# Performance work log

Hardware: AMD Instinct MI355X
Metric: run time of the kernel (lower is better)

Reference implementation:

```python
import jax, jax.numpy as jnp
import numpy as np

N = 100_000      # nodes
E = 1_600_000    # edges
F_IN = 4         # num_features
H = 128          # hidden_channels
C = 5            # num_classes
G = 256          # graphs in batch


def setup_inputs() -> dict:
    key = jax.random.key(0)
    ks = jax.random.split(key, 14)
    x = jax.random.normal(ks[0], (N, F_IN), dtype=jnp.float32)
    edge_index = jax.random.randint(ks[1], (2, E), 0, N, dtype=jnp.int64)
    batch = jnp.sort(jax.random.randint(ks[2], (N,), 0, G, dtype=jnp.int64))
    def lin(k, fan_in, fan_out):
        kw, kb = jax.random.split(k)
        s = 1.0 / np.sqrt(fan_in)
        W = jax.random.uniform(kw, (fan_in, fan_out), jnp.float32, -s, s)
        b = jax.random.uniform(kb, (fan_out,), jnp.float32, -s, s)
        return W, b
    W1, b1 = lin(ks[3], F_IN, H)
    W2, b2 = lin(ks[4], H, H)
    W3, b3 = lin(ks[5], H, H)
    W4, b4 = lin(ks[6], H, H)
    Wl, bl = lin(ks[7], H, C)
    return {"x": x, "edge_index": edge_index, "batch": batch,
            "W1": W1, "b1": b1, "W2": W2, "b2": b2,
            "W3": W3, "b3": b3, "W4": W4, "b4": b4,
            "Wl": Wl, "bl": bl}


def reference(x, edge_index, batch, W1, b1, W2, b2, W3, b3, W4, b4, Wl, bl):
    n = x.shape[0]
    loop = jnp.arange(n, dtype=edge_index.dtype)
    src = jnp.concatenate([edge_index[0], loop])  # [E+N], with self-loops
    dst = jnp.concatenate([edge_index[1], loop])
    # symmetric normalization on A + I (PyG GCNConv default)
    deg = jax.ops.segment_sum(jnp.ones_like(dst, dtype=x.dtype), dst, num_segments=n)
    dinv = deg ** -0.5  # deg >= 1 thanks to self-loops
    coef = dinv[src] * dinv[dst]  # per-edge norm [E+N]

    def conv(h, W, b):
        h = h @ W                               # [N, H]
        msg = h[src] * coef[:, None]            # gather + scale [E+N, H]
        return jax.ops.segment_sum(msg, dst, num_segments=n) + b

    h = jax.nn.relu(conv(x, W1, b1))
    h = jax.nn.relu(conv(h, W2, b2))
    h = jax.nn.relu(conv(h, W3, b3))
    h = jax.nn.relu(conv(h, W4, b4))

    # global_mean_pool over graph ids
    counts = jax.ops.segment_sum(jnp.ones((n,), h.dtype), batch, num_segments=G)
    pooled = jax.ops.segment_sum(h, batch, num_segments=G)
    pooled = pooled / jnp.maximum(counts, 1.0)[:, None]  # [G, H]

    return jax.nn.sigmoid(pooled @ Wl + bl)  # [G, C]
```

## Files before the change

kernel.cpp:

```cpp
#include <hip/hip_runtime.h>
#include <hip/hip_fp8.h>
#include <math.h>

#define N_NODES 100000
#define N_EDGES 1600000
#define F_IN    4
#define HID     128
#define N_CLS   5
#define N_GRAPH 256
#define POOL_SEG 8

#define BSHIFT   9
#define BSIZE    512
#define NBUK     196
#define NCHUNK   200
#define CHUNK    8000

typedef _Float16 f16;
typedef _Float16 f16x2 __attribute__((ext_vector_type(2)));
typedef _Float16 f16x8 __attribute__((ext_vector_type(8)));
typedef float f32x4 __attribute__((ext_vector_type(4)));

__device__ __forceinline__ float rec_coef(unsigned r) {
    return (float)__builtin_bit_cast(_Float16, (unsigned short)(r & 0x7FFFu));
}

__device__ __forceinline__ float2 fp8x2_to_f32x2(unsigned short raw) {
    __hip_fp8x2_e4m3 t;
    t.__x = raw;
    return static_cast<float2>(t);
}

__device__ __forceinline__ void fma8(float c, uint2 v, float* acc) {
    float2 p0 = fp8x2_to_f32x2((unsigned short)(v.x & 0xFFFFu));
    float2 p1 = fp8x2_to_f32x2((unsigned short)(v.x >> 16));
    float2 p2 = fp8x2_to_f32x2((unsigned short)(v.y & 0xFFFFu));
    float2 p3 = fp8x2_to_f32x2((unsigned short)(v.y >> 16));
    acc[0] = fmaf(c, p0.x, acc[0]); acc[1] = fmaf(c, p0.y, acc[1]);
    acc[2] = fmaf(c, p1.x, acc[2]); acc[3] = fmaf(c, p1.y, acc[3]);
    acc[4] = fmaf(c, p2.x, acc[4]); acc[5] = fmaf(c, p2.y, acc[5]);
    acc[6] = fmaf(c, p3.x, acc[6]); acc[7] = fmaf(c, p3.y, acc[7]);
}

__global__ __launch_bounds__(256) void k_bc(const int* __restrict__ dst, int* __restrict__ C) {
    __shared__ int cnt[NBUK];
    int t = threadIdx.x;
    if (t < NBUK) cnt[t] = 0;
    __syncthreads();
    int base = blockIdx.x * CHUNK;
#pragma unroll
    for (int it = 0; it < 32; ++it) {
        int idx = it * 256 + t;
        if (idx < CHUNK) atomicAdd(&cnt[dst[base + idx] >> BSHIFT], 1);
    }
    __syncthreads();
    if (t < NBUK) C[blockIdx.x * NBUK + t] = cnt[t];
}

__global__ __launch_bounds__(256) void k_bscan(const int* __restrict__ C, int* __restrict__ Off,
                                               int* __restrict__ bbase) {
    __shared__ int s[256];
    int b = threadIdx.x;
    int tot = 0;
    if (b < NBUK) {
        for (int c = 0; c < NCHUNK; ++c) {
            Off[c * NBUK + b] = tot;
            tot += C[c * NBUK + b];
        }
    }
    s[b] = (b < NBUK) ? tot : 0;
    __syncthreads();
    for (int off = 1; off < 256; off <<= 1) {
        int v = (b >= off) ? s[b - off] : 0;
        __syncthreads();
        s[b] += v;
        __syncthreads();
    }
    if (b < NBUK) bbase[b] = s[b] - tot;
    if (b == 0) bbase[NBUK] = N_EDGES;
}

__global__ __launch_bounds__(256) void k_scatter(const int* __restrict__ src, const int* __restrict__ dst,
                                                 const int* __restrict__ Off, const int* __restrict__ bbase,
                                                 unsigned* __restrict__ bkt) {
    __shared__ int cur[NBUK];
    int t = threadIdx.x;
    if (t < NBUK) cur[t] = bbase[t] + Off[blockIdx.x * NBUK + t];
    __syncthreads();
    int base = blockIdx.x * CHUNK;
#pragma unroll
    for (int it = 0; it < 32; ++it) {
        int idx = it * 256 + t;
        if (idx < CHUNK) {
            int s = src[base + idx], d = dst[base + idx];
            int b = d >> BSHIFT;
            int p = atomicAdd(&cur[b], 1);
            bkt[p] = ((unsigned)s << BSHIFT) | (unsigned)(d & (BSIZE - 1));
        }
    }
}

__global__ __launch_bounds__(256) void k_hist2(const unsigned* __restrict__ bkt,
                                               const int* __restrict__ bbase,
                                               int* __restrict__ deg, float* __restrict__ dinv,
                                               int* __restrict__ padTot) {
    __shared__ int hist[BSIZE];
    __shared__ int tot;
    int t = threadIdx.x, b = blockIdx.x;
    hist[t] = 0; hist[t + 256] = 0;
    if (t == 0) tot = 0;
    __syncthreads();
    int s0 = bbase[b], s1 = bbase[b + 1];
    for (int e = s0 + t; e < s1; e += 256) atomicAdd(&hist[bkt[e] & (BSIZE - 1)], 1);
    __syncthreads();
    int loc = 0;
#pragma unroll
    for (int h = 0; h < 2; ++h) {
        int l = t + h * 256;
        int node = b * BSIZE + l;
        int d = hist[l];
        if (node < N_NODES) {
            deg[node] = d;
            dinv[node] = rsqrtf((float)d + 1.0f);
        }
        loc += (d + 15) >> 4;
    }
    atomicAdd(&tot, loc);
    __syncthreads();
    if (t == 0) padTot[b] = tot << 4;
}

__global__ __launch_bounds__(256) void k_pscan(const int* __restrict__ padTot, int* __restrict__ padBase,
                                               int* __restrict__ rowptrP) {
    __shared__ int s[256];
    int b = threadIdx.x;
    int v = (b < NBUK) ? padTot[b] : 0;
    s[b] = v;
    __syncthreads();
    for (int off = 1; off < 256; off <<= 1) {
        int u = (b >= off) ? s[b - off] : 0;
        __syncthreads();
        s[b] += u;
        __syncthreads();
    }
    if (b < NBUK) padBase[b] = s[b] - v;
    if (b == 0) {
        padBase[NBUK] = s[NBUK - 1];
        rowptrP[N_NODES] = s[NBUK - 1];
    }
}

__global__ __launch_bounds__(256) void k_local2(const unsigned* __restrict__ bkt,
                                                const int* __restrict__ bbase,
                                                const int* __restrict__ deg,
                                                const float* __restrict__ dinv,
                                                const int* __restrict__ padBase,
                                                int* __restrict__ rowptrP,
                                                unsigned* __restrict__ edges) {
    __shared__ int sc[BSIZE];
    __shared__ int cur[BSIZE];
    __shared__ float dv[BSIZE];
    int t = threadIdx.x, b = blockIdx.x;
    int base = padBase[b];
    int n0 = b * BSIZE + t, n1 = n0 + 256;
    int d0 = (n0 < N_NODES) ? deg[n0] : 0;
    int d1 = (n1 < N_NODES) ? deg[n1] : 0;
    int p0 = ((d0 + 15) >> 4) << 4;
    int p1 = ((d1 + 15) >> 4) << 4;
    sc[t] = p0; sc[t + 256] = p1;
    dv[t] = (n0 < N_NODES) ? dinv[n0] : 0.f;
    dv[t + 256] = (n1 < N_NODES) ? dinv[n1] : 0.f;
    __syncthreads();
    for (int off = 1; off < BSIZE; off <<= 1) {
        int i0 = t, i1 = t + 256;
        int v0 = (i0 >= off) ? sc[i0 - off] : 0;
        int v1 = (i1 >= off) ? sc[i1 - off] : 0;
        __syncthreads();
        sc[i0] += v0; sc[i1] += v1;
        __syncthreads();
    }
    int off0 = base + sc[t] - p0;
    int off1 = base + sc[t + 256] - p1;
    if (n0 < N_NODES) rowptrP[n0] = off0;
    if (n1 < N_NODES) rowptrP[n1] = off1;
    cur[t] = off0; cur[t + 256] = off1;
    int padT = sc[BSIZE - 1];
    for (int i = base + t; i < base + padT; i += 256) edges[i] = 0;
    __syncthreads();
    int s0 = bbase[b], s1 = bbase[b + 1];
    for (int e = s0 + t; e < s1; e += 256) {
        unsigned r = bkt[e];
        int dl = (int)(r & (BSIZE - 1));
        int s = (int)(r >> BSHIFT);
        int p = atomicAdd(&cur[dl], 1);
        float c = dv[dl] * dinv[s];
        unsigned short cb = __builtin_bit_cast(unsigned short, (f16)c);
        edges[p] = ((unsigned)s << 15) | (unsigned)(cb & 0x7FFFu);
    }
}

__global__ __launch_bounds__(256) void k_aggxg(const float4* __restrict__ x,
                                               const int* __restrict__ rowptrP,
                                               const unsigned* __restrict__ edges,
                                               const float* __restrict__ dinv,
                                               const float* __restrict__ W1, const float* __restrict__ b1,
                                               unsigned* __restrict__ hA ) {
    __shared__ float4 sx[256];
    __shared__ float sW[4 * HID];
    __shared__ float sb[HID];
    int tid = threadIdx.x;
    sW[tid] = W1[tid];
    sW[tid + 256] = W1[tid + 256];
    if (tid < HID) sb[tid] = b1[tid];

    int i = blockIdx.x * 256 + tid;
    float4 agg = make_float4(0.f, 0.f, 0.f, 0.f);
    if (i < N_NODES) {
        float di = dinv[i];
        float4 xv = x[i];
        float c0 = di * di;
        agg.x = c0 * xv.x; agg.y = c0 * xv.y; agg.z = c0 * xv.z; agg.w = c0 * xv.w;
        int beg = rowptrP[i], end = rowptrP[i + 1];
        for (int e = beg; e < end; ++e) {
            unsigned r = edges[e];
            float c = rec_coef(r);
            float4 v = x[r >> 15];
            agg.x = fmaf(c, v.x, agg.x); agg.y = fmaf(c, v.y, agg.y);
            agg.z = fmaf(c, v.z, agg.z); agg.w = fmaf(c, v.w, agg.w);
        }
    }
    sx[tid] = agg;
    __syncthreads();

    int node0 = blockIdx.x * 256;
#pragma unroll
    for (int it = 0; it < 32; ++it) {
        int id = it * 256 + tid;
        int n = id >> 5;
        int g = id & 31;
        int node = node0 + n;
        if (node >= N_NODES) continue;
        float4 a = sx[n];
        float c[4];
#pragma unroll
        for (int j = 0; j < 4; ++j) {
            int col = g * 4 + j;
            float v = sb[col];
            v = fmaf(a.x, sW[col],           v);
            v = fmaf(a.y, sW[HID + col],     v);
            v = fmaf(a.z, sW[2 * HID + col], v);
            v = fmaf(a.w, sW[3 * HID + col], v);
            c[j] = fmaxf(v, 0.0f);
        }
        unsigned lo = __hip_fp8x2_e4m3(make_float2(c[0], c[1])).__x;
        unsigned hi = __hip_fp8x2_e4m3(make_float2(c[2], c[3])).__x;
        hA[node * 32 + g] = lo | (hi << 16);
    }
}

__global__ __launch_bounds__(256) void k_agg8p(const unsigned* __restrict__ h8,
                                               const int* __restrict__ rowptrP,
                                               const unsigned* __restrict__ edges,
                                               const float* __restrict__ dinv,
                                               f16* __restrict__ out) {
    int node = blockIdx.x * 4 + (threadIdx.x >> 6);
    if (node >= N_NODES) return;
    int lane = threadIdx.x & 63;
    int g = lane >> 4;
    int l = lane & 15;
    int beg = rowptrP[node], end = rowptrP[node + 1];

    float acc[8];
    {
        float di = dinv[node];
        float c0 = (g == 0) ? di * di : 0.0f;
        uint2 v = *(const uint2*)(h8 + (size_t)node * 32 + l * 2);
        float2 p0 = fp8x2_to_f32x2((unsigned short)(v.x & 0xFFFFu));
        float2 p1 = fp8x2_to_f32x2((unsigned short)(v.x >> 16));
        float2 p2 = fp8x2_to_f32x2((unsigned short)(v.y & 0xFFFFu));
        float2 p3 = fp8x2_to_f32x2((unsigned short)(v.y >> 16));
        acc[0] = c0 * p0.x; acc[1] = c0 * p0.y;
        acc[2] = c0 * p1.x; acc[3] = c0 * p1.y;
        acc[4] = c0 * p2.x; acc[5] = c0 * p2.y;
        acc[6] = c0 * p3.x; acc[7] = c0 * p3.y;
    }

    for (int e = beg; e < end; e += 16) {
        unsigned rec16 = edges[e + l];
#pragma unroll
        for (int i = 0; i < 4; ++i) {
            unsigned rec = __shfl(rec16, i * 4 + g, 64);
            float c = rec_coef(rec);
            uint2 v = *(const uint2*)(h8 + (size_t)(rec >> 15) * 32 + l * 2);
            fma8(c, v, acc);
        }
    }

#pragma unroll
    for (int j = 0; j < 8; ++j) {
        acc[j] += __shfl_xor(acc[j], 16, 64);
        acc[j] += __shfl_xor(acc[j], 32, 64);
    }
    if (lane < 16) {
        f16x8 o;
#pragma unroll
        for (int j = 0; j < 8; ++j) o[j] = (f16)acc[j];
        *(f16x8*)(out + (size_t)node * HID + l * 8) = o;
    }
}

__global__ __launch_bounds__(256) void k_packW3(const float* __restrict__ W2, const float* __restrict__ W3,
                                                const float* __restrict__ W4, f16* __restrict__ Wp) {
    int idx = blockIdx.x * 256 + threadIdx.x;
    int which = idx >> 14;
    int r = idx & 16383;
    const float* W = (which == 0) ? W2 : (which == 1) ? W3 : W4;
    int j  = r & 7;
    int L  = (r >> 3) & 63;
    int ks = (r >> 9) & 3;
    int ct = r >> 11;
    int k = ks * 32 + (L >> 4) * 8 + j;
    int n = ct * 16 + (L & 15);
    Wp[idx] = (f16)W[k * HID + n];
}

template <bool FP8OUT>
__global__ __launch_bounds__(256) void k_gemm_mfma(const f16* __restrict__ A, const f16* __restrict__ Wp,
                                                   const float* __restrict__ bias, void* __restrict__ outv) {
    int wave = threadIdx.x >> 6;
    int lane = threadIdx.x & 63;
    int row0 = blockIdx.x * 64 + wave * 16;
    if (row0 >= N_NODES) return;
    int m = lane & 15;
    int q = lane >> 4;
    const f16* Arow = A + (size_t)(row0 + m) * HID + q * 8;

    f32x4 acc[8];
#pragma unroll
    for (int t = 0; t < 8; ++t) acc[t] = (f32x4){0.f, 0.f, 0.f, 0.f};

#pragma unroll
    for (int ks = 0; ks < 4; ++ks) {
        f16x8 a = *(const f16x8*)(Arow + ks * 32);
#pragma unroll
        for (int t = 0; t < 8; ++t) {
            f16x8 b = *(const f16x8*)(Wp + ((size_t)(t * 4 + ks) * 64 + lane) * 8);
            acc[t] = __builtin_amdgcn_mfma_f32_16x16x32_f16(a, b, acc[t], 0, 0, 0);
        }
    }

    int orow = row0 + q * 4;
#pragma unroll
    for (int t = 0; t < 8; ++t) {
        float bb = bias[t * 16 + m];
#pragma unroll
        for (int r = 0; r < 4; ++r) {
            float val = fmaxf(acc[t][r] + bb, 0.0f);
            if constexpr (FP8OUT) {
                __hip_fp8_e4m3* out8 = (__hip_fp8_e4m3*)outv;
                out8[(size_t)(orow + r) * HID + t * 16 + m] = __hip_fp8_e4m3(val);
            } else {
                f16* out = (f16*)outv;
                out[(size_t)(orow + r) * HID + t * 16 + m] = (f16)val;
            }
        }
    }
}

__device__ __forceinline__ int lower_bound_batch(const int* __restrict__ batch, int val) {
    int lo = 0, hi = N_NODES;
    while (lo < hi) { int m = (lo + hi) >> 1; if (batch[m] < val) lo = m + 1; else hi = m; }
    return lo;
}

__global__ __launch_bounds__(128) void k_pool1(const f16* __restrict__ h, const int* __restrict__ batch,
                                               float* __restrict__ partials) {
    int g = blockIdx.x / POOL_SEG;
    int s = blockIdx.x % POOL_SEG;
    int f = threadIdx.x;
    int beg = lower_bound_batch(batch, g);
    int end = lower_bound_batch(batch, g + 1);
    int len = end - beg;
    int sb = beg + (int)(((long long)len * s) / POOL_SEG);
    int se = beg + (int)(((long long)len * (s + 1)) / POOL_SEG);
    float acc = 0.0f;
    for (int i = sb; i < se; ++i) acc += (float)h[i * HID + f];
    partials[(size_t)blockIdx.x * HID + f] = acc;
}

__global__ __launch_bounds__(128) void k_pool2h(const float* __restrict__ partials,
                                                const int* __restrict__ batch,
                                                const float* __restrict__ Wl, const float* __restrict__ bl,
                                                float* __restrict__ out) {
    __shared__ float sp[HID];
    int g = blockIdx.x;
    int f = threadIdx.x;
    float acc = 0.0f;
#pragma unroll
    for (int s = 0; s < POOL_SEG; ++s)
        acc += partials[(size_t)(g * POOL_SEG + s) * HID + f];
    int beg = lower_bound_batch(batch, g);
    int end = lower_bound_batch(batch, g + 1);
    sp[f] = acc / fmaxf((float)(end - beg), 1.0f);
    __syncthreads();
    if (f < N_CLS) {
        float v = bl[f];
        for (int k = 0; k < HID; ++k) v = fmaf(sp[k], Wl[k * N_CLS + f], v);
        out[g * N_CLS + f] = 1.0f / (1.0f + expf(-v));
    }
}

extern "C" void kernel_launch(void* const* d_in, const int* in_sizes, int n_in,
                              void* d_out, int out_size, void* d_ws, size_t ws_size,
                              hipStream_t stream) {
    const float* x     = (const float*)d_in[0];
    const int*   ei    = (const int*)d_in[1];
    const int*   batch = (const int*)d_in[2];
    const float* W1 = (const float*)d_in[3];  const float* b1 = (const float*)d_in[4];
    const float* W2 = (const float*)d_in[5];  const float* b2 = (const float*)d_in[6];
    const float* W3 = (const float*)d_in[7];  const float* b3 = (const float*)d_in[8];
    const float* W4 = (const float*)d_in[9];  const float* b4 = (const float*)d_in[10];
    const float* Wl = (const float*)d_in[11]; const float* bl = (const float*)d_in[12];
    float* out = (float*)d_out;

    const size_t EPAD = (size_t)N_EDGES + (size_t)N_NODES * 16;

    char* p = (char*)d_ws;
    auto alloc = [&](size_t bytes) { char* r = p; p += (bytes + 255) & ~(size_t)255; return (void*)r; };
    int*      C       = (int*)     alloc((size_t)NCHUNK * NBUK * 4);
    int*      Off     = (int*)     alloc((size_t)NCHUNK * NBUK * 4);
    int*      bbase   = (int*)     alloc((size_t)(NBUK + 1) * 4);
    int*      padTot  = (int*)     alloc((size_t)NBUK * 4);
    int*      padBase = (int*)     alloc((size_t)(NBUK + 1) * 4);
    unsigned* bkt     = (unsigned*)alloc((size_t)N_EDGES * 4);
    int*      deg     = (int*)     alloc((size_t)N_NODES * 4);
    int*      rowptrP = (int*)     alloc((size_t)(N_NODES + 1) * 4);
    float*    dinv    = (float*)   alloc((size_t)N_NODES * 4);
    unsigned* edges   = (unsigned*)alloc(EPAD * 4);
    unsigned* hA      = (unsigned*)alloc((size_t)N_NODES * HID);
    f16*      hB      = (f16*)     alloc((size_t)N_NODES * HID * 2);
    f16*      h4      = (f16*)     alloc((size_t)N_NODES * HID * 2);
    float*    parts   = (float*)   alloc((size_t)N_GRAPH * POOL_SEG * HID * 4);
    f16*      Wp      = (f16*)     alloc((size_t)3 * HID * HID * 2);
    f16*      Wp2 = Wp;
    f16*      Wp3 = Wp + HID * HID;
    f16*      Wp4 = Wp + 2 * HID * HID;

    const int* srcv = ei;
    const int* dstv = ei + N_EDGES;

    const int nb = (N_NODES + 255) / 256;

    k_bc     <<<NCHUNK, 256, 0, stream>>>(dstv, C);
    k_bscan  <<<1, 256, 0, stream>>>(C, Off, bbase);
    k_scatter<<<NCHUNK, 256, 0, stream>>>(srcv, dstv, Off, bbase, bkt);
    k_hist2  <<<NBUK, 256, 0, stream>>>(bkt, bbase, deg, dinv, padTot);
    k_pscan  <<<1, 256, 0, stream>>>(padTot, padBase, rowptrP);
    k_local2 <<<NBUK, 256, 0, stream>>>(bkt, bbase, deg, dinv, padBase, rowptrP, edges);

    k_packW3<<<192, 256, 0, stream>>>(W2, W3, W4, Wp);

    k_aggxg<<<nb, 256, 0, stream>>>((const float4*)x, rowptrP, edges, dinv, W1, b1, hA);

    const int ggrid = (N_NODES + 63) / 64;
    k_agg8p<<<N_NODES / 4, 256, 0, stream>>>(hA, rowptrP, edges, dinv, hB);
    k_gemm_mfma<true ><<<ggrid, 256, 0, stream>>>(hB, Wp2, b2, hA);
    k_agg8p<<<N_NODES / 4, 256, 0, stream>>>(hA, rowptrP, edges, dinv, hB);
    k_gemm_mfma<true ><<<ggrid, 256, 0, stream>>>(hB, Wp3, b3, hA);
    k_agg8p<<<N_NODES / 4, 256, 0, stream>>>(hA, rowptrP, edges, dinv, hB);
    k_gemm_mfma<false><<<ggrid, 256, 0, stream>>>(hB, Wp4, b4, h4);

    k_pool1 <<<N_GRAPH * POOL_SEG, 128, 0, stream>>>(h4, batch, parts);
    k_pool2h<<<N_GRAPH, 128, 0, stream>>>(parts, batch, Wl, bl, out);
}
```

Measured before the change: 377.0 us.

## Fuse GCN aggregation with MFMA GEMM per 16-node block via swizzled LDS

Each hidden layer's sparse aggregation is merged with the following 128x128 MFMA GEMM. A 1024-thread block aggregates 16 nodes (one wave per node) into an XOR-swizzled LDS tile, then 8 waves run the GEMM and write the fp8 or f16 output directly. This removes the fp16 intermediate round trip through global memory and three kernel launches. The first-layer aggregation now uses 16 lanes per node with shuffle reductions instead of one thread per node. The gather address math is also simplified. In exchange, half the waves sit idle during the GEMM phase and the large blocks may limit occupancy.

```diff
diff --git a/kernel.cpp b/kernel.cpp
--- a/kernel.cpp
+++ b/kernel.cpp
@@ -199,48 +199,54 @@
     }
 }
 
-__global__ __launch_bounds__(256) void k_aggxg(const float4* __restrict__ x,
+__global__ __launch_bounds__(256) void k_aggx1(const float4* __restrict__ x,
                                                const int* __restrict__ rowptrP,
                                                const unsigned* __restrict__ edges,
                                                const float* __restrict__ dinv,
                                                const float* __restrict__ W1, const float* __restrict__ b1,
-                                               unsigned* __restrict__ hA ) {
-    __shared__ float4 sx[256];
+                                               unsigned* __restrict__ hA) {
+    __shared__ float4 sxa[16];
     __shared__ float sW[4 * HID];
     __shared__ float sb[HID];
-    int tid = threadIdx.x;
-    sW[tid] = W1[tid];
-    sW[tid + 256] = W1[tid + 256];
-    if (tid < HID) sb[tid] = b1[tid];
-
-    int i = blockIdx.x * 256 + tid;
-    float4 agg = make_float4(0.f, 0.f, 0.f, 0.f);
-    if (i < N_NODES) {
-        float di = dinv[i];
-        float4 xv = x[i];
+    int t = threadIdx.x;
+    sW[t] = W1[t];
+    sW[t + 256] = W1[t + 256];
+    if (t < HID) sb[t] = b1[t];
+    int grp = t >> 4;
+    int l = t & 15;
+    int node = blockIdx.x * 16 + grp;
+    int beg = rowptrP[node], end = rowptrP[node + 1];
+    float ax = 0.f, ay = 0.f, az = 0.f, aw = 0.f;
+    for (int e = beg + l; e < end; e += 16) {
+        unsigned r = edges[e];
+        float c = rec_coef(r);
+        float4 v = x[r >> 15];
+        ax = fmaf(c, v.x, ax); ay = fmaf(c, v.y, ay);
+        az = fmaf(c, v.z, az); aw = fmaf(c, v.w, aw);
+    }
+#pragma unroll
+    for (int off = 1; off < 16; off <<= 1) {
+        ax += __shfl_xor(ax, off, 64);
+        ay += __shfl_xor(ay, off, 64);
+        az += __shfl_xor(az, off, 64);
+        aw += __shfl_xor(aw, off, 64);
+    }
+    if (l == 0) {
+        float di = dinv[node];
         float c0 = di * di;
-        agg.x = c0 * xv.x; agg.y = c0 * xv.y; agg.z = c0 * xv.z; agg.w = c0 * xv.w;
-        int beg = rowptrP[i], end = rowptrP[i + 1];
-        for (int e = beg; e < end; ++e) {
-            unsigned r = edges[e];
-            float c = rec_coef(r);
-            float4 v = x[r >> 15];
-            agg.x = fmaf(c, v.x, agg.x); agg.y = fmaf(c, v.y, agg.y);
-            agg.z = fmaf(c, v.z, agg.z); agg.w = fmaf(c, v.w, agg.w);
-        }
-    }
-    sx[tid] = agg;
-    __syncthreads();
-
-    int node0 = blockIdx.x * 256;
-#pragma unroll
-    for (int it = 0; it < 32; ++it) {
-        int id = it * 256 + tid;
+        float4 xv = x[node];
+        sxa[grp] = make_float4(fmaf(c0, xv.x, ax), fmaf(c0, xv.y, ay),
+                               fmaf(c0, xv.z, az), fmaf(c0, xv.w, aw));
+    }
+    __syncthreads();
+
+    int node0 = blockIdx.x * 16;
+#pragma unroll
+    for (int it = 0; it < 2; ++it) {
+        int id = it * 256 + t;
         int n = id >> 5;
         int g = id & 31;
-        int node = node0 + n;
-        if (node >= N_NODES) continue;
-        float4 a = sx[n];
+        float4 a = sxa[n];
         float c[4];
 #pragma unroll
         for (int j = 0; j < 4; ++j) {
@@ -254,27 +260,33 @@
         }
         unsigned lo = __hip_fp8x2_e4m3(make_float2(c[0], c[1])).__x;
         unsigned hi = __hip_fp8x2_e4m3(make_float2(c[2], c[3])).__x;
-        hA[node * 32 + g] = lo | (hi << 16);
-    }
-}
-
-__global__ __launch_bounds__(256) void k_agg8p(const unsigned* __restrict__ h8,
-                                               const int* __restrict__ rowptrP,
-                                               const unsigned* __restrict__ edges,
-                                               const float* __restrict__ dinv,
-                                               f16* __restrict__ out) {
-    int node = blockIdx.x * 4 + (threadIdx.x >> 6);
-    if (node >= N_NODES) return;
+        hA[(node0 + n) * 32 + g] = lo | (hi << 16);
+    }
+}
+
+template <bool FP8OUT>
+__global__ __launch_bounds__(1024, 8) void k_aggemm8(const unsigned* __restrict__ h8,
+                                                     const int* __restrict__ rowptrP,
+                                                     const unsigned* __restrict__ edges,
+                                                     const float* __restrict__ dinv,
+                                                     const f16* __restrict__ Wp,
+                                                     const float* __restrict__ bias,
+                                                     void* __restrict__ outv) {
+    __shared__ f16 S[16 * HID];
+    int wave = threadIdx.x >> 6;
     int lane = threadIdx.x & 63;
+    int node0 = blockIdx.x * 16;
+    int node = node0 + wave;
     int g = lane >> 4;
     int l = lane & 15;
     int beg = rowptrP[node], end = rowptrP[node + 1];
+    const char* hp = (const char*)h8 + l * 8;
 
     float acc[8];
     {
         float di = dinv[node];
         float c0 = (g == 0) ? di * di : 0.0f;
-        uint2 v = *(const uint2*)(h8 + (size_t)node * 32 + l * 2);
+        uint2 v = *(const uint2*)(hp + ((size_t)node << 7));
         float2 p0 = fp8x2_to_f32x2((unsigned short)(v.x & 0xFFFFu));
         float2 p1 = fp8x2_to_f32x2((unsigned short)(v.x >> 16));
         float2 p2 = fp8x2_to_f32x2((unsigned short)(v.y & 0xFFFFu));
@@ -291,7 +303,7 @@
         for (int i = 0; i < 4; ++i) {
             unsigned rec = __shfl(rec16, i * 4 + g, 64);
             float c = rec_coef(rec);
-            uint2 v = *(const uint2*)(h8 + (size_t)(rec >> 15) * 32 + l * 2);
+            uint2 v = *(const uint2*)(hp + ((rec >> 8) & 0xFFFFFF80u));
             fma8(c, v, acc);
         }
     }
@@ -305,7 +317,34 @@
         f16x8 o;
 #pragma unroll
         for (int j = 0; j < 8; ++j) o[j] = (f16)acc[j];
-        *(f16x8*)(out + (size_t)node * HID + l * 8) = o;
+        int dw = (l * 4) ^ ((wave & 7) << 2);
+        *(f16x8*)&S[wave * HID + dw * 2] = o;
+    }
+    __syncthreads();
+
+    if (wave < 8) {
+        int t = wave;
+        int m = lane & 15;
+        int q = lane >> 4;
+        f32x4 c4 = (f32x4){0.f, 0.f, 0.f, 0.f};
+#pragma unroll
+        for (int ks = 0; ks < 4; ++ks) {
+            int dw = (ks * 16 + q * 4) ^ ((m & 7) << 2);
+            f16x8 a = *(const f16x8*)&S[m * HID + dw * 2];
+            f16x8 b = *(const f16x8*)(Wp + ((size_t)(t * 4 + ks) * 64 + lane) * 8);
+            c4 = __builtin_amdgcn_mfma_f32_16x16x32_f16(a, b, c4, 0, 0, 0);
+        }
+        float bb = bias[t * 16 + m];
+#pragma unroll
+        for (int r = 0; r < 4; ++r) {
+            float val = fmaxf(c4[r] + bb, 0.0f);
+            int row = node0 + q * 4 + r;
+            if constexpr (FP8OUT) {
+                ((__hip_fp8_e4m3*)outv)[(size_t)row * HID + t * 16 + m] = __hip_fp8_e4m3(val);
+            } else {
+                ((f16*)outv)[(size_t)row * HID + t * 16 + m] = (f16)val;
+            }
+        }
     }
 }
 
@@ -324,49 +363,6 @@
     Wp[idx] = (f16)W[k * HID + n];
 }
 
-template <bool FP8OUT>
-__global__ __launch_bounds__(256) void k_gemm_mfma(const f16* __restrict__ A, const f16* __restrict__ Wp,
-                                                   const float* __restrict__ bias, void* __restrict__ outv) {
-    int wave = threadIdx.x >> 6;
-    int lane = threadIdx.x & 63;
-    int row0 = blockIdx.x * 64 + wave * 16;
-    if (row0 >= N_NODES) return;
-    int m = lane & 15;
-    int q = lane >> 4;
-    const f16* Arow = A + (size_t)(row0 + m) * HID + q * 8;
-
-    f32x4 acc[8];
-#pragma unroll
-    for (int t = 0; t < 8; ++t) acc[t] = (f32x4){0.f, 0.f, 0.f, 0.f};
-
-#pragma unroll
-    for (int ks = 0; ks < 4; ++ks) {
-        f16x8 a = *(const f16x8*)(Arow + ks * 32);
-#pragma unroll
-        for (int t = 0; t < 8; ++t) {
-            f16x8 b = *(const f16x8*)(Wp + ((size_t)(t * 4 + ks) * 64 + lane) * 8);
-            acc[t] = __builtin_amdgcn_mfma_f32_16x16x32_f16(a, b, acc[t], 0, 0, 0);
-        }
-    }
-
-    int orow = row0 + q * 4;
-#pragma unroll
-    for (int t = 0; t < 8; ++t) {
-        float bb = bias[t * 16 + m];
-#pragma unroll
-        for (int r = 0; r < 4; ++r) {
-            float val = fmaxf(acc[t][r] + bb, 0.0f);
-            if constexpr (FP8OUT) {
-                __hip_fp8_e4m3* out8 = (__hip_fp8_e4m3*)outv;
-                out8[(size_t)(orow + r) * HID + t * 16 + m] = __hip_fp8_e4m3(val);
-            } else {
-                f16* out = (f16*)outv;
-                out[(size_t)(orow + r) * HID + t * 16 + m] = (f16)val;
-            }
-        }
-    }
-}
-
 __device__ __forceinline__ int lower_bound_batch(const int* __restrict__ batch, int val) {
     int lo = 0, hi = N_NODES;
     while (lo < hi) { int m = (lo + hi) >> 1; if (batch[m] < val) lo = m + 1; else hi = m; }
@@ -438,7 +434,7 @@
     float*    dinv    = (float*)   alloc((size_t)N_NODES * 4);
     unsigned* edges   = (unsigned*)alloc(EPAD * 4);
     unsigned* hA      = (unsigned*)alloc((size_t)N_NODES * HID);
-    f16*      hB      = (f16*)     alloc((size_t)N_NODES * HID * 2);
+    unsigned* hC      = (unsigned*)alloc((size_t)N_NODES * HID);
     f16*      h4      = (f16*)     alloc((size_t)N_NODES * HID * 2);
     float*    parts   = (float*)   alloc((size_t)N_GRAPH * POOL_SEG * HID * 4);
     f16*      Wp      = (f16*)     alloc((size_t)3 * HID * HID * 2);
@@ -449,8 +445,6 @@
     const int* srcv = ei;
     const int* dstv = ei + N_EDGES;
 
-    const int nb = (N_NODES + 255) / 256;
-
     k_bc     <<<NCHUNK, 256, 0, stream>>>(dstv, C);
     k_bscan  <<<1, 256, 0, stream>>>(C, Off, bbase);
     k_scatter<<<NCHUNK, 256, 0, stream>>>(srcv, dstv, Off, bbase, bkt);
@@ -460,15 +454,12 @@
 
     k_packW3<<<192, 256, 0, stream>>>(W2, W3, W4, Wp);
 
-    k_aggxg<<<nb, 256, 0, stream>>>((const float4*)x, rowptrP, edges, dinv, W1, b1, hA);
-
-    const int ggrid = (N_NODES + 63) / 64;
-    k_agg8p<<<N_NODES / 4, 256, 0, stream>>>(hA, rowptrP, edges, dinv, hB);
-    k_gemm_mfma<true ><<<ggrid, 256, 0, stream>>>(hB, Wp2, b2, hA);
-    k_agg8p<<<N_NODES / 4, 256, 0, stream>>>(hA, rowptrP, edges, dinv, hB);
-    k_gemm_mfma<true ><<<ggrid, 256, 0, stream>>>(hB, Wp3, b3, hA);
-    k_agg8p<<<N_NODES / 4, 256, 0, stream>>>(hA, rowptrP, edges, dinv, hB);
-    k_gemm_mfma<false><<<ggrid, 256, 0, stream>>>(hB, Wp4, b4, h4);
+    k_aggx1<<<N_NODES / 16, 256, 0, stream>>>((const float4*)x, rowptrP, edges, dinv, W1, b1, hA);
+
+    const int fgrid = N_NODES / 16;
+    k_aggemm8<true ><<<fgrid, 1024, 0, stream>>>(hA, rowptrP, edges, dinv, Wp2, b2, hC);
+    k_aggemm8<true ><<<fgrid, 1024, 0, stream>>>(hC, rowptrP, edges, dinv, Wp3, b3, hA);
+    k_aggemm8<false><<<fgrid, 1024, 0, stream>>>(hA, rowptrP, edges, dinv, Wp4, b4, h4);
 
     k_pool1 <<<N_GRAPH * POOL_SEG, 128, 0, stream>>>(h4, batch, parts);
     k_pool2h<<<N_GRAPH, 128, 0, stream>>>(parts, batch, Wl, bl, out);
```

New measurement: 357.6 us. 5.2% less time.
